# Performance work log

Measured on AMD Instinct MI355X. Metric: run time of the kernel, lower is better.

## Reference

```python
import jax, jax.numpy as jnp
import numpy as np

EMB = 1024
HEADS = 16
HEAD_DIM = EMB // HEADS
B, S = 4, 2048


def setup_inputs() -> dict:
    key = jax.random.key(0)
    ks = jax.random.split(key, 7)
    sc = 1.0 / np.sqrt(EMB)
    return {
        "query": jax.random.normal(ks[0], (B, S, EMB), jnp.float32),
        "key": jax.random.normal(ks[1], (B, S, EMB), jnp.float32),
        "value": jax.random.normal(ks[2], (B, S, EMB), jnp.float32),
        "Wq": jax.random.normal(ks[3], (EMB, EMB), jnp.float32) * sc,
        "Wk": jax.random.normal(ks[4], (EMB, EMB), jnp.float32) * sc,
        "Wv": jax.random.normal(ks[5], (EMB, EMB), jnp.float32) * sc,
        "Wo": jax.random.normal(ks[6], (EMB, EMB), jnp.float32) * sc,
    }


def reference(query, key, value, Wq, Wk, Wv, Wo):
    # nn.Linear applies x @ W^T; W stored as [out, in]
    def split_heads(x):  # [B,S,E] -> [B,H,S,D]
        return x.reshape(B, -1, HEADS, HEAD_DIM).transpose(0, 2, 1, 3)

    q = split_heads(query @ Wq.T)
    k = split_heads(key @ Wk.T)
    v = split_heads(value @ Wv.T)
    scores = jnp.einsum('bhse,bhte->bhst', q, k) / np.sqrt(HEAD_DIM).astype(np.float32)
    attn = jax.nn.softmax(scores, axis=-1)
    ctx = jnp.einsum('bhst,bhtd->bshd', attn, v)  # [B,S,H,D]
    out = ctx.reshape(B, -1, EMB) @ Wo.T
    return out
```

## Files before the change

### kernel.cpp

```cpp
#include <hip/hip_runtime.h>
#include <hip/hip_bf16.h>

#define EMB   1024
#define HEADS 16
#define HDIM  64
#define BB    4
#define SS    2048
#define MROWS (BB*SS)

typedef __bf16 bf16_t;
typedef __bf16 bf16x4_t __attribute__((ext_vector_type(4)));
typedef __bf16 bf16x8   __attribute__((ext_vector_type(8)));
typedef float  f32x4    __attribute__((ext_vector_type(4)));

__device__ __forceinline__ void glds16(const void* g, void* l) {
  __builtin_amdgcn_global_load_lds(
      (const __attribute__((address_space(1))) void*)g,
      (__attribute__((address_space(3))) void*)l, 16, 0, 0);
}

__launch_bounds__(256)
__global__ void cast_multi(const float* s0, const float* s1, const float* s2,
                           const float* s3, const float* s4, const float* s5,
                           const float* s6,
                           bf16_t* d0, bf16_t* d1, bf16_t* d2, bf16_t* d3,
                           bf16_t* d4, bf16_t* d5, bf16_t* d6, int nact) {
  const int z = blockIdx.z;
  if (z >= nact && blockIdx.x >= 512) return;
  const float* ss[7] = {s0, s1, s2, s3, s4, s5, s6};
  bf16_t*      dd[7] = {d0, d1, d2, d3, d4, d5, d6};
  const float* s = ss[z];
  bf16_t*      d = dd[z];
  const int i = (blockIdx.x*256 + threadIdx.x) * 8;
  const f32x4 a = *(const f32x4*)&s[i];
  const f32x4 b = *(const f32x4*)&s[i+4];
  bf16x8 r;
  r[0]=(bf16_t)a[0]; r[1]=(bf16_t)a[1]; r[2]=(bf16_t)a[2]; r[3]=(bf16_t)a[3];
  r[4]=(bf16_t)b[0]; r[5]=(bf16_t)b[1]; r[6]=(bf16_t)b[2]; r[7]=(bf16_t)b[3];
  *(bf16x8*)&d[i] = r;
}

__launch_bounds__(256)
__global__ void cast_f32_bf16(const float* __restrict__ src, bf16_t* __restrict__ dst) {
  const int i = (blockIdx.x*256 + threadIdx.x) * 8;
  const f32x4 a = *(const f32x4*)&src[i];
  const f32x4 b = *(const f32x4*)&src[i+4];
  bf16x8 r;
  r[0]=(bf16_t)a[0]; r[1]=(bf16_t)a[1]; r[2]=(bf16_t)a[2]; r[3]=(bf16_t)a[3];
  r[4]=(bf16_t)b[0]; r[5]=(bf16_t)b[1]; r[6]=(bf16_t)b[2]; r[7]=(bf16_t)b[3];
  *(bf16x8*)&dst[i] = r;
}

__device__ __forceinline__ void gemm_core(const bf16_t* __restrict__ A,
                                          const bf16_t* __restrict__ W,
                                          bf16_t* As, bf16_t* Bs,
                                          f32x4 acc[4][4],
                                          int bm0, int bn0,
                                          int wave, int lane) {
  const int quad = lane >> 4, l16 = lane & 15;
  const int wm = wave >> 1, wn = wave & 1;
  for (int k0 = 0; k0 < EMB; k0 += 32) {
#pragma unroll
    for (int j = 0; j < 2; ++j) {
      const int i   = wave*2 + j;
      const int row = i*16 + (lane >> 2);
      const int col = (lane & 3) * 8;
      glds16(A + (size_t)(bm0 + row)*EMB + k0 + col, &As[i*512]);
      glds16(W + (size_t)(bn0 + row)*EMB + k0 + col, &Bs[i*512]);
    }
    __syncthreads();

    bf16x8 a[4], b[4];
#pragma unroll
    for (int t = 0; t < 4; ++t) {
      a[t] = *(const bf16x8*)&As[(wm*64 + t*16 + l16)*32 + quad*8];
      b[t] = *(const bf16x8*)&Bs[(wn*64 + t*16 + l16)*32 + quad*8];
    }
#pragma unroll
    for (int mt = 0; mt < 4; ++mt)
#pragma unroll
      for (int nt = 0; nt < 4; ++nt)
        acc[mt][nt] = __builtin_amdgcn_mfma_f32_16x16x32_bf16(a[mt], b[nt], acc[mt][nt], 0, 0, 0);
    __syncthreads();
  }
}

__launch_bounds__(256)
__global__ void gemm_qkv(const bf16_t* A0, const bf16_t* A1, const bf16_t* A2,
                         const bf16_t* W0, const bf16_t* W1, const bf16_t* W2,
                         bf16_t* C0, bf16_t* C1, bf16_t* C2,
                         float sscale, int zbase) {
  __shared__ __align__(16) bf16_t As[128*32];
  __shared__ __align__(16) bf16_t Bs[128*32];
  const int tid  = threadIdx.x;
  const int wave = tid >> 6, lane = tid & 63;
  const int quad = lane >> 4, l16 = lane & 15;
  const int wm = wave >> 1, wn = wave & 1;

  const int fid = blockIdx.x + 8*(blockIdx.y + 64*blockIdx.z);
  const int xcd = fid & 7, s = fid >> 3;
  const int bn0 = (s & 7) * 128;
  const int p   = xcd + 8*(s >> 3);
  const int z   = (p >> 6) + zbase;
  const int bm0 = (p & 63) * 128;

  const bf16_t* A = (z == 0) ? A0 : (z == 1) ? A1 : A2;
  const bf16_t* W = (z == 0) ? W0 : (z == 1) ? W1 : W2;
  bf16_t*       C = (z == 0) ? C0 : (z == 1) ? C1 : C2;
  const float oscale = (z == 0) ? sscale : 1.0f;

  f32x4 acc[4][4] = {};
  gemm_core(A, W, As, Bs, acc, bm0, bn0, wave, lane);

  if (z == 2) {
    const int bb = bm0 >> 11;
    const int T  = ((bm0 & 2047) >> 6) + wm;
    const int h  = (bn0 >> 6) + wn;
    bf16_t* base = C + ((size_t)(bb*HEADS + h)*32 + T)*4096;
#pragma unroll
    for (int ks = 0; ks < 2; ++ks)
#pragma unroll
      for (int nt = 0; nt < 4; ++nt) {
        bf16x8 v;
#pragma unroll
        for (int r = 0; r < 4; ++r) {
          v[r]     = (bf16_t)acc[2*ks][nt][r];
          v[4 + r] = (bf16_t)acc[2*ks + 1][nt][r];
        }
        *(bf16x8*)&base[((nt*2 + ks)*64 + quad*16 + l16)*8] = v;
      }
  } else {
#pragma unroll
    for (int mt = 0; mt < 4; ++mt) {
      const int row = bm0 + wm*64 + mt*16 + quad*4;
#pragma unroll
      for (int nt = 0; nt < 4; ++nt) {
        const int col = bn0 + wn*64 + nt*16 + l16;
#pragma unroll
        for (int r = 0; r < 4; ++r)
          C[(size_t)(row + r)*EMB + col] = (bf16_t)(acc[mt][nt][r] * oscale);
      }
    }
  }
}

__launch_bounds__(256)
__global__ void gemm_out(const bf16_t* __restrict__ A, const bf16_t* __restrict__ W,
                         float* __restrict__ C) {
  __shared__ __align__(16) bf16_t As[64*32];
  __shared__ __align__(16) bf16_t Bs[128*32];
  const int tid  = threadIdx.x;
  const int wave = tid >> 6, lane = tid & 63;
  const int quad = lane >> 4, l16 = lane & 15;
  const int wm = wave >> 1, wn = wave & 1;

  const int fid = blockIdx.x + 8*blockIdx.y;
  const int xcd = fid & 7, s = fid >> 3;
  const int bn0 = (s & 7) * 128;
  const int bm0 = (xcd*16 + (s >> 3)) * 64;

  f32x4 acc[2][4] = {};

  for (int k0 = 0; k0 < EMB; k0 += 32) {
    {
      const int i   = wave;
      const int row = i*16 + (lane >> 2);
      const int col = (lane & 3) * 8;
      glds16(A + (size_t)(bm0 + row)*EMB + k0 + col, &As[i*512]);
    }
#pragma unroll
    for (int j = 0; j < 2; ++j) {
      const int i   = wave*2 + j;
      const int row = i*16 + (lane >> 2);
      const int col = (lane & 3) * 8;
      glds16(W + (size_t)(bn0 + row)*EMB + k0 + col, &Bs[i*512]);
    }
    __syncthreads();

    bf16x8 a[2], b[4];
#pragma unroll
    for (int t2 = 0; t2 < 2; ++t2)
      a[t2] = *(const bf16x8*)&As[(wm*32 + t2*16 + l16)*32 + quad*8];
#pragma unroll
    for (int t2 = 0; t2 < 4; ++t2)
      b[t2] = *(const bf16x8*)&Bs[(wn*64 + t2*16 + l16)*32 + quad*8];
#pragma unroll
    for (int mt = 0; mt < 2; ++mt)
#pragma unroll
      for (int nt = 0; nt < 4; ++nt)
        acc[mt][nt] = __builtin_amdgcn_mfma_f32_16x16x32_bf16(a[mt], b[nt], acc[mt][nt], 0, 0, 0);
    __syncthreads();
  }

#pragma unroll
  for (int mt = 0; mt < 2; ++mt) {
    const int row = bm0 + wm*32 + mt*16 + quad*4;
#pragma unroll
    for (int nt = 0; nt < 4; ++nt) {
      const int col = bn0 + wn*64 + nt*16 + l16;
#pragma unroll
      for (int r = 0; r < 4; ++r)
        C[(size_t)(row + r)*EMB + col] = acc[mt][nt][r];
    }
  }
}

__launch_bounds__(512, 8)
__global__ void attn(const bf16_t* Qp, const bf16_t* __restrict__ Kp,
                     const bf16_t* __restrict__ Vt, bf16_t* Cx) {
  __shared__ __align__(16) bf16_t Ks[2][4096];
  __shared__ __align__(16) bf16_t Vs[3][4096];

  const int tid  = threadIdx.x;
  const int wave = tid >> 6, lane = tid & 63;
  const int quad = lane >> 4, l16 = lane & 15;

  const int fid  = blockIdx.x + 16*(blockIdx.y + 16*blockIdx.z);
  const int xcd  = fid & 7, s = fid >> 3;
  const int q0   = (s & 15) * 128;
  const int pair = xcd*8 + (s >> 4);
  const int h    = pair & 15;
  const int b    = pair >> 4;

  bf16x8 qf[2];
  {
    const size_t qr = (size_t)(b*SS + q0 + wave*16 + l16)*EMB + h*HDIM;
    qf[0] = *(const bf16x8*)&Qp[qr + quad*8];
    qf[1] = *(const bf16x8*)&Qp[qr + 32 + quad*8];
  }

  const bf16_t* Kb = Kp + (size_t)b*SS*EMB + h*HDIM;
  const bf16_t* Vb = Vt + ((size_t)(b*HEADS + h)*32)*4096;

  f32x4 o[4] = {};
  f32x4 lsv = {};
  bf16x8 pb[2];

  auto stage = [&](int ti, int kbuf, int vbuf) {
    const int t0 = ti * 64;
    const int i  = wave;
    glds16(Kb + (size_t)(t0 + (i&3)*16 + l16)*EMB + (i>>2)*32 + quad*8,
           &Ks[kbuf][i*512]);
    glds16(Vb + (size_t)ti*4096 + i*512 + lane*8, &Vs[vbuf][i*512]);
  };

  auto QK = [&](int bf, f32x4 (&st)[4]) {
#pragma unroll
    for (int cb = 0; cb < 4; ++cb) {
      const bf16x8 kf0 = *(const bf16x8*)&Ks[bf][cb*512 + lane*8];
      const bf16x8 kf1 = *(const bf16x8*)&Ks[bf][2048 + cb*512 + lane*8];
      st[cb] = __builtin_amdgcn_mfma_f32_16x16x32_bf16(kf0, qf[0], st[cb], 0, 0, 0);
      st[cb] = __builtin_amdgcn_mfma_f32_16x16x32_bf16(kf1, qf[1], st[cb], 0, 0, 0);
    }
  };

  auto SM = [&](f32x4 (&st)[4]) {
#pragma unroll
    for (int kb = 0; kb < 4; ++kb) {
#pragma unroll
      for (int r = 0; r < 4; ++r)
        st[kb][r] = __builtin_amdgcn_exp2f(st[kb][r]);
      lsv += st[kb];
    }
#pragma unroll
    for (int ks = 0; ks < 2; ++ks)
#pragma unroll
      for (int r = 0; r < 4; ++r) {
        pb[ks][r]     = (bf16_t)st[2*ks][r];
        pb[ks][4 + r] = (bf16_t)st[2*ks + 1][r];
      }
  };

  auto PV = [&](int bf) {
#pragma unroll
    for (int ks = 0; ks < 2; ++ks)
#pragma unroll
      for (int dt = 0; dt < 4; ++dt) {
        const bf16x8 vf = *(const bf16x8*)&Vs[bf][((dt*2 + ks)*64 + lane)*8];
        o[dt] = __builtin_amdgcn_mfma_f32_16x16x32_bf16(vf, pb[ks], o[dt], 0, 0, 0);
      }
  };

  stage(0, 0, 0);
  __syncthreads();
  stage(1, 1, 1);
  {
    f32x4 st[4] = {};
    QK(0, st);
    SM(st);
  }

  const int NT = SS / 64;
  int vr = 0;
  int vw = 2;
  for (int t = 0; t < NT - 1; ++t) {
    __syncthreads();
    if (t + 2 < NT) stage(t + 2, t & 1, vw);
    __builtin_amdgcn_s_setprio(1);
    f32x4 stn[4] = {};
    QK((t + 1) & 1, stn);
    PV(vr);
    __builtin_amdgcn_s_setprio(0);
    SM(stn);
    vr = (vr == 2) ? 0 : vr + 1;
    vw = (vw == 2) ? 0 : vw + 1;
  }

  PV(vr);

  float l = lsv[0] + lsv[1] + lsv[2] + lsv[3];
  l += __shfl_xor(l, 16, 64);
  l += __shfl_xor(l, 32, 64);
  const float inv = 1.0f / l;
  const size_t row = (size_t)(b*SS + q0 + wave*16 + l16)*EMB + h*HDIM;
#pragma unroll
  for (int dt = 0; dt < 4; ++dt) {
    bf16x4_t v;
#pragma unroll
    for (int r = 0; r < 4; ++r) v[r] = (bf16_t)(o[dt][r] * inv);
    *(bf16x4_t*)&Cx[row + dt*16 + quad*4] = v;
  }
}

extern "C" void kernel_launch(void* const* d_in, const int* in_sizes, int n_in,
                              void* d_out, int out_size, void* d_ws, size_t ws_size,
                              hipStream_t stream) {
  (void)in_sizes; (void)n_in; (void)out_size;
  const float* query = (const float*)d_in[0];
  const float* key   = (const float*)d_in[1];
  const float* value = (const float*)d_in[2];
  const float* WqF   = (const float*)d_in[3];
  const float* WkF   = (const float*)d_in[4];
  const float* WvF   = (const float*)d_in[5];
  const float* WoF   = (const float*)d_in[6];

  const size_t AN = (size_t)MROWS*EMB;
  const size_t WN = (size_t)EMB*EMB;
  float* out = (float*)d_out;
  bf16_t* S5 = (bf16_t*)d_out;
  bf16_t* S6 = S5 + AN;

  const float sscale = 0.125f * 1.44269504f;

  const dim3 gqkv(EMB/128, MROWS/128, 3);
  const dim3 gqk (EMB/128, MROWS/128, 2);
  const dim3 gv  (EMB/128, MROWS/128, 1);
  const dim3 gg  (8, 128);
  const dim3 gattn(SS/128, HEADS, BB);

  if (ws_size >= (size_t)(4*AN + 4*WN) * sizeof(bf16_t)) {
    bf16_t* qb  = (bf16_t*)d_ws;
    bf16_t* kb  = qb + AN;
    bf16_t* vb  = kb + AN;
    bf16_t* S2  = vb + AN;
    bf16_t* Wqb = S2 + AN;
    bf16_t* Wkb = Wqb + WN;
    bf16_t* Wvb = Wkb + WN;
    bf16_t* Wob = Wvb + WN;

    cast_multi<<<dim3(AN/2048, 1, 7), 256, 0, stream>>>(
        query, key, value, WqF, WkF, WvF, WoF,
        qb, kb, vb, Wqb, Wkb, Wvb, Wob, 3);
    gemm_qkv<<<gqkv, 256, 0, stream>>>(qb, kb, vb, Wqb, Wkb, Wvb,
                                       S2, S6, S5, sscale, 0);
    attn<<<gattn, 512, 0, stream>>>(S2, S6, S5, S2);
    gemm_out<<<gg, 256, 0, stream>>>(S2, Wob, out);
  } else {
    bf16_t* S1  = (bf16_t*)d_ws;
    bf16_t* S2  = S1 + AN;
    bf16_t* Wqb = S2 + AN;
    bf16_t* Wkb = Wqb + WN;
    bf16_t* Wvb = Wkb + WN;
    bf16_t* Wob = Wvb + WN;

    cast_multi<<<dim3(AN/2048, 1, 6), 256, 0, stream>>>(
        query, key, WqF, WkF, WvF, WoF, WoF,
        S1, S5, Wqb, Wkb, Wvb, Wob, Wob, 2);
    gemm_qkv<<<gqk, 256, 0, stream>>>(S1, S5, S1, Wqb, Wkb, Wvb,
                                      S2, S6, S5, sscale, 0);
    cast_f32_bf16<<<dim3(AN/2048), 256, 0, stream>>>(value, S1);
    gemm_qkv<<<gv, 256, 0, stream>>>(S1, S1, S1, Wvb, Wvb, Wvb,
                                     S5, S5, S5, 1.0f, 2);
    attn<<<gattn, 512, 0, stream>>>(S2, S6, S5, S2);
    gemm_out<<<gg, 256, 0, stream>>>(S2, Wob, out);
  }
}
```

Baseline: 314.9 us.

## Process two 16-row query tiles per wave in attention with 256-thread blocks

The attention kernel now runs 4 waves per block instead of 8, and each wave handles 32 query rows (two 16-row MFMA tiles) instead of 16. Each K and V fragment read from LDS is reused for two MFMAs, which halves LDS read traffic per unit of compute. Staging issues two global-to-LDS loads per wave to keep the tile size the same. In exchange, register use per wave roughly doubles for accumulators and score tiles, there are fewer waves to hide latency, and the launch bound occupancy hint drops.

Result: no change. 320.8 us (+1.9%).

```diff
diff --git a/kernel.cpp b/kernel.cpp
--- a/kernel.cpp
+++ b/kernel.cpp
@@ -205,7 +205,7 @@
   }
 }
 
-__launch_bounds__(512, 8)
+__launch_bounds__(256, 4)
 __global__ void attn(const bf16_t* Qp, const bf16_t* __restrict__ Kp,
                      const bf16_t* __restrict__ Vt, bf16_t* Cx) {
   __shared__ __align__(16) bf16_t Ks[2][4096];
@@ -222,53 +222,63 @@
   const int h    = pair & 15;
   const int b    = pair >> 4;
 
-  bf16x8 qf[2];
-  {
-    const size_t qr = (size_t)(b*SS + q0 + wave*16 + l16)*EMB + h*HDIM;
-    qf[0] = *(const bf16x8*)&Qp[qr + quad*8];
-    qf[1] = *(const bf16x8*)&Qp[qr + 32 + quad*8];
+  bf16x8 qf[2][2];
+#pragma unroll
+  for (int mb = 0; mb < 2; ++mb) {
+    const size_t qr = (size_t)(b*SS + q0 + wave*32 + mb*16 + l16)*EMB + h*HDIM;
+    qf[mb][0] = *(const bf16x8*)&Qp[qr + quad*8];
+    qf[mb][1] = *(const bf16x8*)&Qp[qr + 32 + quad*8];
   }
 
   const bf16_t* Kb = Kp + (size_t)b*SS*EMB + h*HDIM;
   const bf16_t* Vb = Vt + ((size_t)(b*HEADS + h)*32)*4096;
 
-  f32x4 o[4] = {};
-  f32x4 lsv = {};
-  bf16x8 pb[2];
+  f32x4 o[2][4] = {};
+  f32x4 lsv[2] = {};
+  bf16x8 pb[2][2];
 
   auto stage = [&](int ti, int kbuf, int vbuf) {
     const int t0 = ti * 64;
-    const int i  = wave;
-    glds16(Kb + (size_t)(t0 + (i&3)*16 + l16)*EMB + (i>>2)*32 + quad*8,
-           &Ks[kbuf][i*512]);
-    glds16(Vb + (size_t)ti*4096 + i*512 + lane*8, &Vs[vbuf][i*512]);
+#pragma unroll
+    for (int c = 0; c < 2; ++c) {
+      const int i = wave + c*4;
+      glds16(Kb + (size_t)(t0 + (i&3)*16 + l16)*EMB + (i>>2)*32 + quad*8,
+             &Ks[kbuf][i*512]);
+      glds16(Vb + (size_t)ti*4096 + i*512 + lane*8, &Vs[vbuf][i*512]);
+    }
   };
 
-  auto QK = [&](int bf, f32x4 (&st)[4]) {
+  auto QK = [&](int bf, f32x4 (&st)[2][4]) {
 #pragma unroll
     for (int cb = 0; cb < 4; ++cb) {
       const bf16x8 kf0 = *(const bf16x8*)&Ks[bf][cb*512 + lane*8];
       const bf16x8 kf1 = *(const bf16x8*)&Ks[bf][2048 + cb*512 + lane*8];
-      st[cb] = __builtin_amdgcn_mfma_f32_16x16x32_bf16(kf0, qf[0], st[cb], 0, 0, 0);
-      st[cb] = __builtin_amdgcn_mfma_f32_16x16x32_bf16(kf1, qf[1], st[cb], 0, 0, 0);
+#pragma unroll
+      for (int mb = 0; mb < 2; ++mb) {
+        st[mb][cb] = __builtin_amdgcn_mfma_f32_16x16x32_bf16(kf0, qf[mb][0], st[mb][cb], 0, 0, 0);
+        st[mb][cb] = __builtin_amdgcn_mfma_f32_16x16x32_bf16(kf1, qf[mb][1], st[mb][cb], 0, 0, 0);
+      }
     }
   };
 
-  auto SM = [&](f32x4 (&st)[4]) {
-#pragma unroll
-    for (int kb = 0; kb < 4; ++kb) {
-#pragma unroll
-      for (int r = 0; r < 4; ++r)
-        st[kb][r] = __builtin_amdgcn_exp2f(st[kb][r]);
-      lsv += st[kb];
-    }
-#pragma unroll
-    for (int ks = 0; ks < 2; ++ks)
-#pragma unroll
-      for (int r = 0; r < 4; ++r) {
-        pb[ks][r]     = (bf16_t)st[2*ks][r];
-        pb[ks][4 + r] = (bf16_t)st[2*ks + 1][r];
+  auto SM = [&](f32x4 (&st)[2][4]) {
+#pragma unroll
+    for (int mb = 0; mb < 2; ++mb) {
+#pragma unroll
+      for (int kb = 0; kb < 4; ++kb) {
+#pragma unroll
+        for (int r = 0; r < 4; ++r)
+          st[mb][kb][r] = __builtin_amdgcn_exp2f(st[mb][kb][r]);
+        lsv[mb] += st[mb][kb];
       }
+#pragma unroll
+      for (int ks = 0; ks < 2; ++ks)
+#pragma unroll
+        for (int r = 0; r < 4; ++r) {
+          pb[mb][ks][r]     = (bf16_t)st[mb][2*ks][r];
+          pb[mb][ks][4 + r] = (bf16_t)st[mb][2*ks + 1][r];
+        }
+    }
   };
 
   auto PV = [&](int bf) {
@@ -277,7 +287,9 @@
 #pragma unroll
       for (int dt = 0; dt < 4; ++dt) {
         const bf16x8 vf = *(const bf16x8*)&Vs[bf][((dt*2 + ks)*64 + lane)*8];
-        o[dt] = __builtin_amdgcn_mfma_f32_16x16x32_bf16(vf, pb[ks], o[dt], 0, 0, 0);
+#pragma unroll
+        for (int mb = 0; mb < 2; ++mb)
+          o[mb][dt] = __builtin_amdgcn_mfma_f32_16x16x32_bf16(vf, pb[mb][ks], o[mb][dt], 0, 0, 0);
       }
   };
 
@@ -285,7 +297,7 @@
   __syncthreads();
   stage(1, 1, 1);
   {
-    f32x4 st[4] = {};
+    f32x4 st[2][4] = {};
     QK(0, st);
     SM(st);
   }
@@ -297,7 +309,7 @@
     __syncthreads();
     if (t + 2 < NT) stage(t + 2, t & 1, vw);
     __builtin_amdgcn_s_setprio(1);
-    f32x4 stn[4] = {};
+    f32x4 stn[2][4] = {};
     QK((t + 1) & 1, stn);
     PV(vr);
     __builtin_amdgcn_s_setprio(0);
@@ -308,17 +320,20 @@
 
   PV(vr);
 
-  float l = lsv[0] + lsv[1] + lsv[2] + lsv[3];
-  l += __shfl_xor(l, 16, 64);
-  l += __shfl_xor(l, 32, 64);
-  const float inv = 1.0f / l;
-  const size_t row = (size_t)(b*SS + q0 + wave*16 + l16)*EMB + h*HDIM;
-#pragma unroll
-  for (int dt = 0; dt < 4; ++dt) {
-    bf16x4_t v;
-#pragma unroll
-    for (int r = 0; r < 4; ++r) v[r] = (bf16_t)(o[dt][r] * inv);
-    *(bf16x4_t*)&Cx[row + dt*16 + quad*4] = v;
+#pragma unroll
+  for (int mb = 0; mb < 2; ++mb) {
+    float l = lsv[mb][0] + lsv[mb][1] + lsv[mb][2] + lsv[mb][3];
+    l += __shfl_xor(l, 16, 64);
+    l += __shfl_xor(l, 32, 64);
+    const float inv = 1.0f / l;
+    const size_t row = (size_t)(b*SS + q0 + wave*32 + mb*16 + l16)*EMB + h*HDIM;
+#pragma unroll
+    for (int dt = 0; dt < 4; ++dt) {
+      bf16x4_t v;
+#pragma unroll
+      for (int r = 0; r < 4; ++r) v[r] = (bf16_t)(o[mb][dt][r] * inv);
+      *(bf16x4_t*)&Cx[row + dt*16 + quad*4] = v;
+    }
   }
 }
 
@@ -363,7 +378,7 @@
         qb, kb, vb, Wqb, Wkb, Wvb, Wob, 3);
     gemm_qkv<<<gqkv, 256, 0, stream>>>(qb, kb, vb, Wqb, Wkb, Wvb,
                                        S2, S6, S5, sscale, 0);
-    attn<<<gattn, 512, 0, stream>>>(S2, S6, S5, S2);
+    attn<<<gattn, 256, 0, stream>>>(S2, S6, S5, S2);
     gemm_out<<<gg, 256, 0, stream>>>(S2, Wob, out);
   } else {
     bf16_t* S1  = (bf16_t*)d_ws;
@@ -381,7 +396,7 @@
     cast_f32_bf16<<<dim3(AN/2048), 256, 0, stream>>>(value, S1);
     gemm_qkv<<<gv, 256, 0, stream>>>(S1, S1, S1, Wvb, Wvb, Wvb,
                                      S5, S5, S5, 1.0f, 2);
-    attn<<<gattn, 512, 0, stream>>>(S2, S6, S5, S2);
+    attn<<<gattn, 256, 0, stream>>>(S2, S6, S5, S2);
     gemm_out<<<gg, 256, 0, stream>>>(S2, Wob, out);
   }
 }
```
